# Optimization experiments

Measured on AMD Instinct MI355X. Metric: run time of the kernel, lower is better.

The kernel has to match this reference:

```python
import jax, jax.numpy as jnp
import numpy as np

N_HEAD = 8
D_K = 64
D_V = 512
TOP_K = 64
NEG = jnp.finfo(jnp.float32).min


def setup_inputs() -> dict:
    key = jax.random.key(0)
    ks = jax.random.split(key, 10)
    B, Lq, Lk, E = 2, 2048, 2048, 512
    q = jax.random.normal(ks[0], (B, Lq, E), dtype=jnp.float32)
    k = jax.random.normal(ks[1], (B, Lk, E), dtype=jnp.float32)
    v = jax.random.normal(ks[2], (B, Lk, D_V), dtype=jnp.float32)
    post_softmax_mask = jax.random.randint(ks[3], (B, 1, Lq, Lk), 0, 2, dtype=jnp.int32)
    query_mask_flat = jax.random.uniform(ks[4], (B, Lq), dtype=jnp.float32)
    # Linear weights stored input-major: y = x @ W
    Wq = jax.random.normal(ks[5], (E, N_HEAD * D_K), dtype=jnp.float32) * (E ** -0.5)
    Wk = jax.random.normal(ks[6], (E, N_HEAD * D_K), dtype=jnp.float32) * (E ** -0.5)
    Wv = jax.random.normal(ks[7], (D_V, N_HEAD * D_V), dtype=jnp.float32) * (D_V ** -0.5)
    Wfc = jax.random.normal(ks[8], (N_HEAD * D_V, D_V), dtype=jnp.float32) * ((N_HEAD * D_V) ** -0.5)
    return {"q": q, "k": k, "v": v, "post_softmax_mask": post_softmax_mask,
            "query_mask_flat": query_mask_flat, "Wq": Wq, "Wk": Wk, "Wv": Wv, "Wfc": Wfc}


def _topk_keep_mask(logits, top_k):
    # Scatter True at the per-row top-k indices (matches torch.topk + scatter_).
    B, H, Lq, Lk = logits.shape
    _, idx = jax.lax.top_k(logits, top_k)              # [B,H,Lq,K]
    rows = B * H * Lq
    keep = jnp.zeros((rows, Lk), dtype=bool)
    keep = keep.at[jnp.arange(rows)[:, None], idx.reshape(rows, top_k)].set(True)
    return keep.reshape(B, H, Lq, Lk)


def reference(q, k, v, post_softmax_mask, query_mask_flat, Wq, Wk, Wv, Wfc):
    B, Lq, _ = q.shape
    Lk = k.shape[1]
    q_proj = (q @ Wq).reshape(B, Lq, N_HEAD, D_K).transpose(0, 2, 1, 3)   # [B,H,Lq,dk]
    k_proj = (k @ Wk).reshape(B, Lk, N_HEAD, D_K).transpose(0, 2, 1, 3)   # [B,H,Lk,dk]
    logits = jnp.einsum('bhqd,bhkd->bhqk', q_proj * (D_K ** -0.5), k_proj).astype(jnp.float32)
    # post-softmax mask (applied pre-softmax via -inf fill, as in source)
    logits = jnp.where(post_softmax_mask == 0, NEG, logits)
    # top-k restriction, skipped for rows where query_mask_flat <= 0.5
    keep = _topk_keep_mask(logits, TOP_K)
    masked_queries = (query_mask_flat > 0.5)[:, None, :, None]            # [B,1,Lq,1]
    keep = jnp.where(masked_queries, keep, True)
    logits = jnp.where(keep, logits, NEG)
    attn_probs = jax.nn.softmax(logits, axis=-1).astype(v.dtype)          # [B,H,Lq,Lk]
    v_proj = (v @ Wv).reshape(B, Lk, N_HEAD, D_V).transpose(0, 2, 1, 3)   # [B,H,Lk,dv]
    mixed = jnp.einsum('bhqk,bhkd->bhqd', attn_probs, v_proj)
    output = mixed.transpose(0, 2, 1, 3).reshape(B, Lq, N_HEAD * D_V) @ Wfc
    return output, attn_probs
```

## Files before the change

kernel.cpp:

```cpp
#include <hip/hip_runtime.h>
#include <stdint.h>

#define NEGF  (-3.402823466e38f)
#define TOPK  64

typedef __attribute__((ext_vector_type(8))) short bfrag8;
typedef __attribute__((ext_vector_type(4))) float f32x4;
typedef __attribute__((ext_vector_type(16))) float f32x16;

static __device__ __forceinline__ unsigned short f2bf(float f) {
  union { float f; unsigned u; } c; c.f = f;
  unsigned u = c.u;
  return (unsigned short)((u + 0x7fffu + ((u >> 16) & 1u)) >> 16);
}
static __device__ __forceinline__ unsigned mono(float x) {
  union { float f; unsigned u; } c; c.f = x;
  return (c.u & 0x80000000u) ? ~c.u : (c.u | 0x80000000u);
}
static __device__ __forceinline__ float invmono(unsigned k) {
  union { unsigned u; float f; } c;
  c.u = (k & 0x80000000u) ? (k ^ 0x80000000u) : ~k;
  return c.f;
}
static __device__ __forceinline__ int waveSum(int v) {
  #pragma unroll
  for (int o = 1; o < 64; o <<= 1) v += __shfl_xor(v, o);
  return v;
}
static __device__ __forceinline__ float waveSumF(float v) {
  #pragma unroll
  for (int o = 1; o < 64; o <<= 1) v += __shfl_xor(v, o);
  return v;
}
static __device__ __forceinline__ unsigned waveMaxU(unsigned v) {
  #pragma unroll
  for (int o = 1; o < 64; o <<= 1) {
    unsigned t = (unsigned)__shfl_xor((int)v, o);
    v = v > t ? v : t;
  }
  return v;
}

template<int OBF>
__global__ __launch_bounds__(256) void transpose_k(const float* __restrict__ in,
                                                   void* __restrict__ out, int R, int C) {
  __shared__ float t[32][33];
  int c0 = blockIdx.x * 32, r0 = blockIdx.y * 32;
  int tx = threadIdx.x & 31, ty = (threadIdx.x >> 5) * 4;
  #pragma unroll
  for (int i = 0; i < 4; i++)
    t[ty + i][tx] = in[(size_t)(r0 + ty + i) * C + c0 + tx];
  __syncthreads();
  #pragma unroll
  for (int i = 0; i < 4; i++) {
    float v = t[tx][ty + i];
    size_t idx = (size_t)(c0 + ty + i) * R + r0 + tx;
    if (OBF) ((unsigned short*)out)[idx] = f2bf(v);
    else     ((float*)out)[idx] = v;
  }
}

__global__ __launch_bounds__(256) void proj_f32_kernel(
    const float* __restrict__ q, const float* __restrict__ k,
    const float* __restrict__ WqT, const float* __restrict__ WkT,
    float* __restrict__ qp, float* __restrict__ kp) {
  __shared__ float AsT[64][132];
  __shared__ float BsT[64][132];
  int tid = threadIdx.x;
  int z = blockIdx.z;
  const float* A  = z ? k : q;
  const float* Bt = z ? WkT : WqT;
  float* out      = z ? kp : qp;
  float scale     = z ? 1.0f : 0.125f;
  int m0 = blockIdx.y * 128, n0 = blockIdx.x * 128;
  int lane = tid & 63, w = tid >> 6;
  int lx = lane & 15, ly = lane >> 4;
  int ra = w * 32 + ly * 4;
  int ca = lx * 4;
  int rr = tid >> 1;
  int kq0 = (tid & 1) << 5;
  float acc[8][8] = {};
  for (int k0 = 0; k0 < 512; k0 += 64) {
    const float* ar = A  + (size_t)(m0 + rr) * 512 + k0 + kq0;
    const float* br = Bt + (size_t)(n0 + rr) * 512 + k0 + kq0;
    #pragma unroll
    for (int s = 0; s < 8; s++) {
      float4 av = *(const float4*)(ar + (s << 2));
      float4 bv = *(const float4*)(br + (s << 2));
      int kk = kq0 + (s << 2);
      AsT[kk+0][rr] = av.x; AsT[kk+1][rr] = av.y; AsT[kk+2][rr] = av.z; AsT[kk+3][rr] = av.w;
      BsT[kk+0][rr] = bv.x; BsT[kk+1][rr] = bv.y; BsT[kk+2][rr] = bv.z; BsT[kk+3][rr] = bv.w;
    }
    __syncthreads();
    #pragma unroll 2
    for (int d = 0; d < 64; d++) {
      f32x4 a0 = *(const f32x4*)&AsT[d][ra];
      f32x4 a1 = *(const f32x4*)&AsT[d][ra + 16];
      f32x4 b0 = *(const f32x4*)&BsT[d][ca];
      f32x4 b1 = *(const f32x4*)&BsT[d][ca + 64];
      float a[8] = {a0[0],a0[1],a0[2],a0[3],a1[0],a1[1],a1[2],a1[3]};
      float bb[8] = {b0[0],b0[1],b0[2],b0[3],b1[0],b1[1],b1[2],b1[3]};
      #pragma unroll
      for (int i = 0; i < 8; i++)
        #pragma unroll
        for (int j = 0; j < 8; j++)
          acc[i][j] = fmaf(a[i], bb[j], acc[i][j]);
    }
    __syncthreads();
  }
  #pragma unroll
  for (int i = 0; i < 8; i++) {
    int m = m0 + ra + (i & 3) + ((i >> 2) << 4);
    int b = m >> 11, l = m & 2047;
    #pragma unroll
    for (int half = 0; half < 2; half++) {
      int n = n0 + ca + half * 64;
      int h = n >> 6, dd = n & 63;
      float4 v4;
      v4.x = acc[i][half*4+0]*scale; v4.y = acc[i][half*4+1]*scale;
      v4.z = acc[i][half*4+2]*scale; v4.w = acc[i][half*4+3]*scale;
      *(float4*)(out + ((((size_t)b*8 + h)*2048 + l)*64 + dd)) = v4;
    }
  }
}

__global__ __launch_bounds__(256) void logits_mask_kernel(
    const float* __restrict__ qp, const float* __restrict__ kp,
    const int* __restrict__ mask, float* __restrict__ out) {
  __shared__ float AsT[64][132];
  __shared__ float BsT[64][132];
  int tid = threadIdx.x;
  int z = blockIdx.z, b = z >> 3;
  int m0 = blockIdx.y * 128, n0 = blockIdx.x * 128;
  const float* Ap = qp + (size_t)z * (2048 * 64);
  const float* Bp = kp + (size_t)z * (2048 * 64);
  {
    int rr = tid >> 2;
    int kq = (tid & 3) << 2;
    #pragma unroll
    for (int pass = 0; pass < 2; pass++) {
      int r = rr + (pass << 6);
      const float* ar = Ap + (size_t)(m0 + r) * 64 + kq;
      const float* br = Bp + (size_t)(n0 + r) * 64 + kq;
      #pragma unroll
      for (int s = 0; s < 4; s++) {
        float4 av = *(const float4*)(ar + (s << 4));
        float4 bv = *(const float4*)(br + (s << 4));
        int k = kq + (s << 4);
        AsT[k+0][r] = av.x; AsT[k+1][r] = av.y; AsT[k+2][r] = av.z; AsT[k+3][r] = av.w;
        BsT[k+0][r] = bv.x; BsT[k+1][r] = bv.y; BsT[k+2][r] = bv.z; BsT[k+3][r] = bv.w;
      }
    }
  }
  __syncthreads();
  int lane = tid & 63, w = tid >> 6;
  int lx = lane & 15, ly = lane >> 4;
  int ra = w * 32 + ly * 4;
  int ca = lx * 4;
  float acc[8][8] = {};
  #pragma unroll 2
  for (int d = 0; d < 64; d++) {
    f32x4 a0 = *(const f32x4*)&AsT[d][ra];
    f32x4 a1 = *(const f32x4*)&AsT[d][ra + 16];
    f32x4 b0 = *(const f32x4*)&BsT[d][ca];
    f32x4 b1 = *(const f32x4*)&BsT[d][ca + 64];
    float a[8] = {a0[0],a0[1],a0[2],a0[3],a1[0],a1[1],a1[2],a1[3]};
    float bb[8] = {b0[0],b0[1],b0[2],b0[3],b1[0],b1[1],b1[2],b1[3]};
    #pragma unroll
    for (int i = 0; i < 8; i++)
      #pragma unroll
      for (int j = 0; j < 8; j++)
        acc[i][j] = fmaf(a[i], bb[j], acc[i][j]);
  }
  size_t outbase = (size_t)z * 2048 * 2048;
  const int* mbase = mask + (size_t)b * 2048 * 2048;
  #pragma unroll
  for (int i = 0; i < 8; i++) {
    int row = m0 + ra + (i & 3) + ((i >> 2) << 4);
    const int* mp = mbase + (size_t)row * 2048 + n0;
    float* op = out + outbase + (size_t)row * 2048 + n0;
    int4 mv0 = *(const int4*)(mp + ca);
    int4 mv1 = *(const int4*)(mp + ca + 64);
    float4 o0, o1;
    o0.x = mv0.x ? acc[i][0] : NEGF;
    o0.y = mv0.y ? acc[i][1] : NEGF;
    o0.z = mv0.z ? acc[i][2] : NEGF;
    o0.w = mv0.w ? acc[i][3] : NEGF;
    o1.x = mv1.x ? acc[i][4] : NEGF;
    o1.y = mv1.y ? acc[i][5] : NEGF;
    o1.z = mv1.z ? acc[i][6] : NEGF;
    o1.w = mv1.w ? acc[i][7] : NEGF;
    *(float4*)(op + ca) = o0;
    *(float4*)(op + ca + 64) = o1;
  }
}

__global__ __launch_bounds__(256) void vproj_kernel(const float* __restrict__ v,
    const unsigned short* __restrict__ WvT, unsigned short* __restrict__ vpT) {
  __shared__ unsigned short As[128][64];
  __shared__ unsigned short Bs[128][64];
  int tid = threadIdx.x;
  int lane = tid & 63, wv = tid >> 6;
  int l31 = lane & 31, lh = lane >> 5;
  int wr = wv >> 1, wc = wv & 1;
  int z = blockIdx.z, b = z >> 3, h = z & 7;
  int m0 = blockIdx.y * 128, n0 = blockIdx.x * 128;
  const unsigned short* Ap = WvT + (size_t)(h * 512 + m0) * 512;
  const float* Bp = v + ((size_t)b * 2048 + n0) * 512;
  f32x16 acc[2][2];
  #pragma unroll
  for (int mf = 0; mf < 2; mf++)
    #pragma unroll
    for (int nf = 0; nf < 2; nf++)
      #pragma unroll
      for (int r = 0; r < 16; r++) acc[mf][nf][r] = 0.f;
  int srow = tid >> 1;
  int skc = (tid & 1) << 5;
  for (int k0 = 0; k0 < 512; k0 += 64) {
    {
      const bfrag8* s = (const bfrag8*)(Ap + (size_t)srow * 512 + k0 + skc);
      #pragma unroll
      for (int j = 0; j < 4; j++) {
        int c = (skc >> 3) + j;
        *(bfrag8*)&As[srow][((c + srow) & 7) * 8] = s[j];
      }
    }
    {
      const float* s = Bp + (size_t)srow * 512 + k0 + skc;
      #pragma unroll
      for (int j = 0; j < 4; j++) {
        float4 x0 = *(const float4*)(s + 8*j);
        float4 x1 = *(const float4*)(s + 8*j + 4);
        union { bfrag8 v; unsigned short u[8]; } p;
        p.u[0]=f2bf(x0.x); p.u[1]=f2bf(x0.y); p.u[2]=f2bf(x0.z); p.u[3]=f2bf(x0.w);
        p.u[4]=f2bf(x1.x); p.u[5]=f2bf(x1.y); p.u[6]=f2bf(x1.z); p.u[7]=f2bf(x1.w);
        int c = (skc >> 3) + j;
        *(bfrag8*)&Bs[srow][((c + srow) & 7) * 8] = p.v;
      }
    }
    __syncthreads();
    #pragma unroll
    for (int ks = 0; ks < 4; ks++) {
      int qd = ks * 2 + lh;
      bfrag8 af[2], bfr[2];
      #pragma unroll
      for (int mf = 0; mf < 2; mf++) {
        int r = wr * 64 + mf * 32 + l31;
        af[mf] = *(const bfrag8*)&As[r][((qd + r) & 7) * 8];
      }
      #pragma unroll
      for (int nf = 0; nf < 2; nf++) {
        int n = wc * 64 + nf * 32 + l31;
        bfr[nf] = *(const bfrag8*)&Bs[n][((qd + n) & 7) * 8];
      }
      #pragma unroll
      for (int mf = 0; mf < 2; mf++)
        #pragma unroll
        for (int nf = 0; nf < 2; nf++)
          acc[mf][nf] = __builtin_amdgcn_mfma_f32_32x32x16_bf16(af[mf], bfr[nf], acc[mf][nf], 0, 0, 0);
    }
    __syncthreads();
  }
  #pragma unroll
  for (int mf = 0; mf < 2; mf++)
    #pragma unroll
    for (int nf = 0; nf < 2; nf++) {
      int l = n0 + wc * 64 + nf * 32 + l31;
      #pragma unroll
      for (int r = 0; r < 16; r++) {
        int d = m0 + wr * 64 + mf * 32 + (r & 3) + ((r >> 2) << 3) + (lh << 2);
        vpT[((size_t)z * 512 + d) * 2048 + l] = f2bf(acc[mf][nf][r]);
      }
    }
}

__global__ __launch_bounds__(256) void gemm_bf16_fc(const unsigned short* __restrict__ A,
    const unsigned short* __restrict__ Bt, float* __restrict__ Cout,
    int M, int N, int K) {
  __shared__ unsigned short As[64][72];
  __shared__ unsigned short Bs[128][72];
  int tid = threadIdx.x;
  int lane = tid & 63, wave = tid >> 6;
  int wr = wave >> 1, wc = wave & 1;
  int m0 = blockIdx.y * 64, n0 = blockIdx.x * 128;
  f32x4 acc[2][4];
  #pragma unroll
  for (int mi = 0; mi < 2; mi++)
    #pragma unroll
    for (int ni = 0; ni < 4; ni++) acc[mi][ni] = (f32x4){0.f, 0.f, 0.f, 0.f};
  int arow = tid >> 2, akc = (tid & 3) << 4;
  int brow = tid >> 1, bkc = (tid & 1) << 5;
  for (int k0 = 0; k0 < K; k0 += 64) {
    {
      const bfrag8* s = (const bfrag8*)(A + (size_t)(m0 + arow) * K + k0 + akc);
      *(bfrag8*)&As[arow][akc + 0] = s[0];
      *(bfrag8*)&As[arow][akc + 8] = s[1];
    }
    {
      const bfrag8* s = (const bfrag8*)(Bt + (size_t)(n0 + brow) * K + k0 + bkc);
      #pragma unroll
      for (int j = 0; j < 4; j++)
        *(bfrag8*)&Bs[brow][bkc + 8*j] = s[j];
    }
    __syncthreads();
    #pragma unroll
    for (int kh = 0; kh < 2; kh++) {
      int krd = (kh << 5) + ((lane >> 4) << 3);
      bfrag8 af[2], bfr[4];
      #pragma unroll
      for (int mi = 0; mi < 2; mi++)
        af[mi] = *(const bfrag8*)&As[wr*32 + mi*16 + (lane & 15)][krd];
      #pragma unroll
      for (int ni = 0; ni < 4; ni++)
        bfr[ni] = *(const bfrag8*)&Bs[wc*64 + ni*16 + (lane & 15)][krd];
      #pragma unroll
      for (int mi = 0; mi < 2; mi++)
        #pragma unroll
        for (int ni = 0; ni < 4; ni++)
          acc[mi][ni] = __builtin_amdgcn_mfma_f32_16x16x32_bf16(af[mi], bfr[ni], acc[mi][ni], 0, 0, 0);
    }
    __syncthreads();
  }
  #pragma unroll
  for (int mi = 0; mi < 2; mi++) {
    int rb = m0 + wr*32 + mi*16 + ((lane >> 4) << 2);
    #pragma unroll
    for (int ni = 0; ni < 4; ni++) {
      int col = n0 + wc*64 + ni*16 + (lane & 15);
      f32x4 v = acc[mi][ni];
      #pragma unroll
      for (int j = 0; j < 4; j++)
        Cout[(size_t)(rb + j)*512 + col] = v[j];
    }
  }
}

__global__ __launch_bounds__(512) void pv_kernel(const float* __restrict__ probs,
    const unsigned short* __restrict__ vpT, unsigned short* __restrict__ mixed) {
  __shared__ unsigned short As[64][64];
  __shared__ unsigned short Bs[512][64];
  int tid = threadIdx.x;
  int lane = tid & 63, wv = tid >> 6;
  int l31 = lane & 31, lh = lane >> 5;
  int z = blockIdx.z, m0 = blockIdx.y * 64;
  const float* Ap = probs + (size_t)z * 2048 * 2048 + (size_t)m0 * 2048;
  const unsigned short* Bp = vpT + (size_t)z * 512 * 2048;
  f32x16 acc[2][2];
  #pragma unroll
  for (int mf = 0; mf < 2; mf++)
    #pragma unroll
    for (int nf = 0; nf < 2; nf++)
      #pragma unroll
      for (int r = 0; r < 16; r++) acc[mf][nf][r] = 0.f;
  int a_r = tid >> 3, a_c = tid & 7;
  for (int k0 = 0; k0 < 2048; k0 += 64) {
    {
      const float* s = Ap + (size_t)a_r * 2048 + k0 + a_c * 8;
      float4 x0 = *(const float4*)s;
      float4 x1 = *(const float4*)(s + 4);
      union { bfrag8 v; unsigned short u[8]; } p;
      p.u[0]=f2bf(x0.x); p.u[1]=f2bf(x0.y); p.u[2]=f2bf(x0.z); p.u[3]=f2bf(x0.w);
      p.u[4]=f2bf(x1.x); p.u[5]=f2bf(x1.y); p.u[6]=f2bf(x1.z); p.u[7]=f2bf(x1.w);
      *(bfrag8*)&As[a_r][((a_c + a_r) & 7) * 8] = p.v;
    }
    #pragma unroll
    for (int s = 0; s < 8; s++) {
      int n = (tid >> 3) + (s << 6);
      bfrag8 vb = *(const bfrag8*)(Bp + (size_t)n * 2048 + k0 + a_c * 8);
      *(bfrag8*)&Bs[n][((a_c + n) & 7) * 8] = vb;
    }
    __syncthreads();
    #pragma unroll
    for (int ks = 0; ks < 4; ks++) {
      int qd = ks * 2 + lh;
      bfrag8 af[2], bfr[2];
      #pragma unroll
      for (int mf = 0; mf < 2; mf++) {
        int r = mf * 32 + l31;
        af[mf] = *(const bfrag8*)&As[r][((qd + r) & 7) * 8];
      }
      #pragma unroll
      for (int nf = 0; nf < 2; nf++) {
        int n = wv * 64 + nf * 32 + l31;
        bfr[nf] = *(const bfrag8*)&Bs[n][((qd + n) & 7) * 8];
      }
      #pragma unroll
      for (int mf = 0; mf < 2; mf++)
        #pragma unroll
        for (int nf = 0; nf < 2; nf++)
          acc[mf][nf] = __builtin_amdgcn_mfma_f32_32x32x16_bf16(af[mf], bfr[nf], acc[mf][nf], 0, 0, 0);
    }
    __syncthreads();
  }
  int bb = z >> 3, h = z & 7;
  #pragma unroll
  for (int mf = 0; mf < 2; mf++)
    #pragma unroll
    for (int nf = 0; nf < 2; nf++) {
      int n = wv * 64 + nf * 32 + l31;
      #pragma unroll
      for (int r = 0; r < 16; r++) {
        int row = m0 + mf * 32 + (r & 3) + ((r >> 2) << 3) + (lh << 2);
        mixed[((size_t)bb * 2048 + row) * 4096 + h * 512 + n] = f2bf(acc[mf][nf][r]);
      }
    }
}

__global__ __launch_bounds__(256) void topk_softmax_k(float* __restrict__ probs,
    const float* __restrict__ qmaskf) {
  int lane = threadIdx.x & 63;
  int row = blockIdx.x * 4 + (threadIdx.x >> 6);
  int b = row >> 14, q = row & 2047;
  float* rp = probs + (size_t)row * 2048;
  unsigned key[32];
  #pragma unroll
  for (int j = 0; j < 8; j++) {
    int base = (lane << 2) + (j << 8);
    float4 v = *(const float4*)(rp + base);
    key[4*j+0] = mono(v.x);
    key[4*j+1] = mono(v.y);
    key[4*j+2] = mono(v.z);
    key[4*j+3] = mono(v.w);
  }
  unsigned drop = 0;
  bool qm = qmaskf[b * 2048 + q] > 0.5f;
  if (qm) {
    unsigned lo = 0u, hi = 0xFFFFu;
    while (lo < hi) {
      unsigned mid = lo + ((hi - lo + 1u) >> 1);
      unsigned t = mid << 16;
      int c = 0;
      #pragma unroll
      for (int e = 0; e < 32; e++) c += (key[e] >= t) ? 1 : 0;
      c = waveSum(c);
      if (c >= TOPK) lo = mid; else hi = mid - 1u;
    }
    unsigned P = lo;
    unsigned hiMax = (P << 16) | 0xFFFFu;
    int cgt_hi = 0;
    #pragma unroll
    for (int e = 0; e < 32; e++) cgt_hi += (key[e] > hiMax) ? 1 : 0;
    cgt_hi = waveSum(cgt_hi);
    int remaining = TOPK - cgt_hi;
    unsigned cur = 0xFFFFFFFFu;
    unsigned K64 = P << 16;
    for (;;) {
      unsigned mx = 0;
      #pragma unroll
      for (int e = 0; e < 32; e++) {
        unsigned kk = key[e];
        if ((kk >> 16) == P && kk < cur) mx = mx > kk ? mx : kk;
      }
      mx = waveMaxU(mx);
      int ce = 0;
      #pragma unroll
      for (int e = 0; e < 32; e++) ce += (key[e] == mx) ? 1 : 0;
      ce = waveSum(ce);
      if (remaining <= ce) { K64 = mx; break; }
      remaining -= ce;
      cur = mx;
    }
    int cgt = 0, ceq = 0;
    #pragma unroll
    for (int e = 0; e < 32; e++) { cgt += (key[e] > K64) ? 1 : 0; ceq += (key[e] == K64) ? 1 : 0; }
    cgt = waveSum(cgt);
    int ceqT = waveSum(ceq);
    int r = TOPK - cgt;
    #pragma unroll
    for (int e = 0; e < 32; e++) if (key[e] < K64) drop |= (1u << e);
    if (ceqT > r) {
      int taken = 0;
      for (int j = 0; j < 8; j++) {
        int cl = 0, eqm = 0;
        #pragma unroll
        for (int t = 0; t < 4; t++)
          if (key[4*j+t] == K64) { eqm |= (1 << t); cl++; }
        int incl = cl;
        for (int o = 1; o < 64; o <<= 1) {
          int tt = __shfl_up(incl, o);
          if (lane >= o) incl += tt;
        }
        int pref = incl - cl;
        int tot = __shfl(incl, 63);
        int rk = taken + pref;
        #pragma unroll
        for (int t = 0; t < 4; t++) {
          if ((eqm >> t) & 1) {
            if (rk >= r) drop |= (1u << (4*j+t));
            rk++;
          }
        }
        taken += tot;
      }
    }
  }
  unsigned kmax = 0;
  #pragma unroll
  for (int e = 0; e < 32; e++)
    if (!((drop >> e) & 1u)) kmax = kmax > key[e] ? kmax : key[e];
  kmax = waveMaxU(kmax);
  float mx = invmono(kmax);
  float ex[32]; float s = 0.f;
  #pragma unroll
  for (int e = 0; e < 32; e++) {
    float t = ((drop >> e) & 1u) ? 0.f : __expf(invmono(key[e]) - mx);
    ex[e] = t; s += t;
  }
  s = waveSumF(s);
  float inv = 1.0f / s;
  #pragma unroll
  for (int j = 0; j < 8; j++) {
    int base = (lane << 2) + (j << 8);
    float4 o;
    o.x = ex[4*j+0]*inv; o.y = ex[4*j+1]*inv; o.z = ex[4*j+2]*inv; o.w = ex[4*j+3]*inv;
    *(float4*)(rp + base) = o;
  }
}

extern "C" void kernel_launch(void* const* d_in, const int* in_sizes, int n_in,
                              void* d_out, int out_size, void* d_ws, size_t ws_size,
                              hipStream_t stream) {
  (void)in_sizes; (void)n_in; (void)out_size; (void)ws_size;
  const float* q     = (const float*)d_in[0];
  const float* k     = (const float*)d_in[1];
  const float* v     = (const float*)d_in[2];
  const int*   mask  = (const int*)d_in[3];
  const float* qmask = (const float*)d_in[4];
  const float* Wq    = (const float*)d_in[5];
  const float* Wk    = (const float*)d_in[6];
  const float* Wv    = (const float*)d_in[7];
  const float* Wfc   = (const float*)d_in[8];

  float* out   = (float*)d_out;
  float* probs = out + 2097152;

  char* ws = (char*)d_ws;
  float*          qp    = (float*)(ws + 0);
  float*          kp    = (float*)(ws + 8388608);
  unsigned short* vpT   = (unsigned short*)(ws + 16777216);
  unsigned short* mixed = (unsigned short*)(ws + 50331648);
  float*          WqT   = (float*)(ws + 83886080);
  float*          WkT   = (float*)(ws + 84934656);
  unsigned short* WvT   = (unsigned short*)(ws + 85983232);
  unsigned short* WfcT  = (unsigned short*)(ws + 90177536);

  transpose_k<0><<<dim3(16, 16),  256, 0, stream>>>(Wq,  WqT,  512, 512);
  transpose_k<0><<<dim3(16, 16),  256, 0, stream>>>(Wk,  WkT,  512, 512);
  transpose_k<1><<<dim3(128, 16), 256, 0, stream>>>(Wv,  WvT,  512, 4096);
  transpose_k<1><<<dim3(16, 128), 256, 0, stream>>>(Wfc, WfcT, 4096, 512);

  proj_f32_kernel<<<dim3(4, 32, 2), 256, 0, stream>>>(q, k, WqT, WkT, qp, kp);

  vproj_kernel<<<dim3(16, 4, 16), 256, 0, stream>>>(v, WvT, vpT);

  logits_mask_kernel<<<dim3(16, 16, 16), 256, 0, stream>>>(qp, kp, mask, probs);

  topk_softmax_k<<<dim3(8192), 256, 0, stream>>>(probs, qmask);

  pv_kernel<<<dim3(1, 32, 16), 512, 0, stream>>>(probs, vpT, mixed);

  gemm_bf16_fc<<<dim3(4, 64), 256, 0, stream>>>(mixed, WfcT, out, 4096, 512, 4096);
}
```

Measured before the change: 581.0 us.

## Fuse logits, mask, top-k and softmax into one kernel; remap PV blocks per XCD

Replaces the separate logits+mask kernel and the top-k/softmax kernel with one ltk_kernel. Each block computes full 2048-wide logit rows for 32 queries from a transposed K held in double-buffered LDS, then does the top-k selection and softmax in registers. This removes one full write and read of the 2048x2048x16 float logits tensor in HBM. It also uses ballot/popcount counts, packed bf16 conversion, a reworked FMA loop in the projection, and an XCD-aware block remap for pv_kernel. The cost is a new kpT transpose pass, heavy register pressure (128 logit values per thread) and large shared-memory use, which may limit occupancy.

```diff
diff --git a/kernel.cpp b/kernel.cpp
--- a/kernel.cpp
+++ b/kernel.cpp
@@ -13,6 +13,11 @@
   unsigned u = c.u;
   return (unsigned short)((u + 0x7fffu + ((u >> 16) & 1u)) >> 16);
 }
+static __device__ __forceinline__ unsigned cvtpk_bf16(float lo, float hi) {
+  unsigned r;
+  asm("v_cvt_pk_bf16_f32 %0, %1, %2" : "=v"(r) : "v"(lo), "v"(hi));
+  return r;
+}
 static __device__ __forceinline__ unsigned mono(float x) {
   union { float f; unsigned u; } c; c.f = x;
   return (c.u & 0x80000000u) ? ~c.u : (c.u | 0x80000000u);
@@ -21,11 +26,6 @@
   union { unsigned u; float f; } c;
   c.u = (k & 0x80000000u) ? (k ^ 0x80000000u) : ~k;
   return c.f;
-}
-static __device__ __forceinline__ int waveSum(int v) {
-  #pragma unroll
-  for (int o = 1; o < 64; o <<= 1) v += __shfl_xor(v, o);
-  return v;
 }
 static __device__ __forceinline__ float waveSumF(float v) {
   #pragma unroll
@@ -58,6 +58,23 @@
     if (OBF) ((unsigned short*)out)[idx] = f2bf(v);
     else     ((float*)out)[idx] = v;
   }
+}
+
+__global__ __launch_bounds__(256) void transpose_kp_kernel(const float* __restrict__ kp,
+    float* __restrict__ kpT) {
+  __shared__ float t[32][33];
+  int z = blockIdx.z;
+  const float* in = kp + (size_t)z * 2048 * 64;
+  float* out = kpT + (size_t)z * 64 * 2048;
+  int c0 = blockIdx.x * 32, r0 = blockIdx.y * 32;
+  int tx = threadIdx.x & 31, ty = (threadIdx.x >> 5) * 4;
+  #pragma unroll
+  for (int i = 0; i < 4; i++)
+    t[ty + i][tx] = in[(size_t)(r0 + ty + i) * 64 + c0 + tx];
+  __syncthreads();
+  #pragma unroll
+  for (int i = 0; i < 4; i++)
+    out[(size_t)(c0 + ty + i) * 2048 + r0 + tx] = t[tx][ty + i];
 }
 
 __global__ __launch_bounds__(256) void proj_f32_kernel(
@@ -92,19 +109,22 @@
       BsT[kk+0][rr] = bv.x; BsT[kk+1][rr] = bv.y; BsT[kk+2][rr] = bv.z; BsT[kk+3][rr] = bv.w;
     }
     __syncthreads();
-    #pragma unroll 2
+    #pragma unroll 4
     for (int d = 0; d < 64; d++) {
       f32x4 a0 = *(const f32x4*)&AsT[d][ra];
       f32x4 a1 = *(const f32x4*)&AsT[d][ra + 16];
       f32x4 b0 = *(const f32x4*)&BsT[d][ca];
       f32x4 b1 = *(const f32x4*)&BsT[d][ca + 64];
-      float a[8] = {a0[0],a0[1],a0[2],a0[3],a1[0],a1[1],a1[2],a1[3]};
-      float bb[8] = {b0[0],b0[1],b0[2],b0[3],b1[0],b1[1],b1[2],b1[3]};
-      #pragma unroll
-      for (int i = 0; i < 8; i++)
-        #pragma unroll
-        for (int j = 0; j < 8; j++)
-          acc[i][j] = fmaf(a[i], bb[j], acc[i][j]);
+      #pragma unroll
+      for (int i = 0; i < 4; i++) {
+        #pragma unroll
+        for (int j = 0; j < 4; j++) {
+          acc[i][j]     = fmaf(a0[i], b0[j], acc[i][j]);
+          acc[i][j+4]   = fmaf(a0[i], b1[j], acc[i][j+4]);
+          acc[i+4][j]   = fmaf(a1[i], b0[j], acc[i+4][j]);
+          acc[i+4][j+4] = fmaf(a1[i], b1[j], acc[i+4][j+4]);
+        }
+      }
     }
     __syncthreads();
   }
@@ -124,74 +144,153 @@
   }
 }
 
-__global__ __launch_bounds__(256) void logits_mask_kernel(
-    const float* __restrict__ qp, const float* __restrict__ kp,
-    const int* __restrict__ mask, float* __restrict__ out) {
-  __shared__ float AsT[64][132];
-  __shared__ float BsT[64][132];
+__global__ __launch_bounds__(512, 2) void ltk_kernel(
+    const float* __restrict__ qp, const float* __restrict__ kpT,
+    const int* __restrict__ mask, const float* __restrict__ qmaskf,
+    float* __restrict__ probs) {
+  __shared__ float As[32][68];
+  __shared__ float Bs[2][4 * 2048];
   int tid = threadIdx.x;
-  int z = blockIdx.z, b = z >> 3;
-  int m0 = blockIdx.y * 128, n0 = blockIdx.x * 128;
+  int lane = tid & 63, w = tid >> 6;
+  int z = blockIdx.y, b = z >> 3;
+  int m0 = blockIdx.x * 32;
   const float* Ap = qp + (size_t)z * (2048 * 64);
-  const float* Bp = kp + (size_t)z * (2048 * 64);
+  const float* Bp = kpT + (size_t)z * (64 * 2048);
   {
-    int rr = tid >> 2;
-    int kq = (tid & 3) << 2;
-    #pragma unroll
-    for (int pass = 0; pass < 2; pass++) {
-      int r = rr + (pass << 6);
-      const float* ar = Ap + (size_t)(m0 + r) * 64 + kq;
-      const float* br = Bp + (size_t)(n0 + r) * 64 + kq;
-      #pragma unroll
-      for (int s = 0; s < 4; s++) {
-        float4 av = *(const float4*)(ar + (s << 4));
-        float4 bv = *(const float4*)(br + (s << 4));
-        int k = kq + (s << 4);
-        AsT[k+0][r] = av.x; AsT[k+1][r] = av.y; AsT[k+2][r] = av.z; AsT[k+3][r] = av.w;
-        BsT[k+0][r] = bv.x; BsT[k+1][r] = bv.y; BsT[k+2][r] = bv.z; BsT[k+3][r] = bv.w;
-      }
-    }
-  }
-  __syncthreads();
-  int lane = tid & 63, w = tid >> 6;
-  int lx = lane & 15, ly = lane >> 4;
-  int ra = w * 32 + ly * 4;
-  int ca = lx * 4;
-  float acc[8][8] = {};
-  #pragma unroll 2
-  for (int d = 0; d < 64; d++) {
-    f32x4 a0 = *(const f32x4*)&AsT[d][ra];
-    f32x4 a1 = *(const f32x4*)&AsT[d][ra + 16];
-    f32x4 b0 = *(const f32x4*)&BsT[d][ca];
-    f32x4 b1 = *(const f32x4*)&BsT[d][ca + 64];
-    float a[8] = {a0[0],a0[1],a0[2],a0[3],a1[0],a1[1],a1[2],a1[3]};
-    float bb[8] = {b0[0],b0[1],b0[2],b0[3],b1[0],b1[1],b1[2],b1[3]};
-    #pragma unroll
-    for (int i = 0; i < 8; i++)
-      #pragma unroll
-      for (int j = 0; j < 8; j++)
-        acc[i][j] = fmaf(a[i], bb[j], acc[i][j]);
-  }
-  size_t outbase = (size_t)z * 2048 * 2048;
-  const int* mbase = mask + (size_t)b * 2048 * 2048;
-  #pragma unroll
-  for (int i = 0; i < 8; i++) {
-    int row = m0 + ra + (i & 3) + ((i >> 2) << 4);
-    const int* mp = mbase + (size_t)row * 2048 + n0;
-    float* op = out + outbase + (size_t)row * 2048 + n0;
-    int4 mv0 = *(const int4*)(mp + ca);
-    int4 mv1 = *(const int4*)(mp + ca + 64);
-    float4 o0, o1;
-    o0.x = mv0.x ? acc[i][0] : NEGF;
-    o0.y = mv0.y ? acc[i][1] : NEGF;
-    o0.z = mv0.z ? acc[i][2] : NEGF;
-    o0.w = mv0.w ? acc[i][3] : NEGF;
-    o1.x = mv1.x ? acc[i][4] : NEGF;
-    o1.y = mv1.y ? acc[i][5] : NEGF;
-    o1.z = mv1.z ? acc[i][6] : NEGF;
-    o1.w = mv1.w ? acc[i][7] : NEGF;
-    *(float4*)(op + ca) = o0;
-    *(float4*)(op + ca + 64) = o1;
+    int r = tid >> 4, c4 = (tid & 15) << 2;
+    *(f32x4*)&As[r][c4] = *(const f32x4*)(Ap + (size_t)(m0 + r) * 64 + c4);
+  }
+  int sdd = tid >> 7, sc = (tid & 127) << 2;
+  {
+    #pragma unroll
+    for (int s = 0; s < 4; s++)
+      *(f32x4*)&Bs[0][sdd * 2048 + sc + 512 * s] =
+          *(const f32x4*)(Bp + (size_t)sdd * 2048 + sc + 512 * s);
+  }
+  float lg[4][32];
+  #pragma unroll
+  for (int r = 0; r < 4; r++)
+    #pragma unroll
+    for (int j = 0; j < 32; j++) lg[r][j] = 0.f;
+  int buf = 0;
+  for (int it = 0; it < 16; ++it) {
+    __syncthreads();
+    f32x4 pre0, pre1, pre2, pre3;
+    if (it < 15) {
+      const float* s = Bp + (size_t)(4 * (it + 1) + sdd) * 2048 + sc;
+      pre0 = *(const f32x4*)(s);
+      pre1 = *(const f32x4*)(s + 512);
+      pre2 = *(const f32x4*)(s + 1024);
+      pre3 = *(const f32x4*)(s + 1536);
+    }
+    f32x4 a0 = *(const f32x4*)&As[4*w+0][it * 4];
+    f32x4 a1 = *(const f32x4*)&As[4*w+1][it * 4];
+    f32x4 a2 = *(const f32x4*)&As[4*w+2][it * 4];
+    f32x4 a3 = *(const f32x4*)&As[4*w+3][it * 4];
+    const float* Bb = &Bs[buf][0];
+    #pragma unroll
+    for (int j = 0; j < 32; ++j) {
+      int col = lane + 64 * j;
+      float b0 = Bb[col], b1 = Bb[2048 + col], b2 = Bb[4096 + col], b3 = Bb[6144 + col];
+      lg[0][j] = fmaf(a0[3], b3, fmaf(a0[2], b2, fmaf(a0[1], b1, fmaf(a0[0], b0, lg[0][j]))));
+      lg[1][j] = fmaf(a1[3], b3, fmaf(a1[2], b2, fmaf(a1[1], b1, fmaf(a1[0], b0, lg[1][j]))));
+      lg[2][j] = fmaf(a2[3], b3, fmaf(a2[2], b2, fmaf(a2[1], b1, fmaf(a2[0], b0, lg[2][j]))));
+      lg[3][j] = fmaf(a3[3], b3, fmaf(a3[2], b2, fmaf(a3[1], b1, fmaf(a3[0], b0, lg[3][j]))));
+    }
+    if (it < 15) {
+      float* d = &Bs[buf ^ 1][sdd * 2048 + sc];
+      *(f32x4*)(d)        = pre0;
+      *(f32x4*)(d + 512)  = pre1;
+      *(f32x4*)(d + 1024) = pre2;
+      *(f32x4*)(d + 1536) = pre3;
+    }
+    buf ^= 1;
+  }
+  int bbase = b * 2048;
+  #pragma unroll
+  for (int r = 0; r < 4; ++r) {
+    int row = m0 + 4 * w + r;
+    const int* mp = mask + ((size_t)bbase + row) * 2048;
+    unsigned key[32];
+    #pragma unroll
+    for (int j = 0; j < 32; ++j) {
+      int mm = mp[lane + 64 * j];
+      key[j] = mono(mm ? lg[r][j] : NEGF);
+    }
+    bool qm = qmaskf[bbase + row] > 0.5f;
+    unsigned drop = 0;
+    if (qm) {
+      unsigned lo = 0u, hi = 0xFFFFu;
+      while (lo < hi) {
+        unsigned mid = lo + ((hi - lo + 1u) >> 1);
+        unsigned t = mid << 16;
+        int c = 0;
+        #pragma unroll
+        for (int e = 0; e < 32; e++) c += __popcll(__ballot(key[e] >= t));
+        if (c >= TOPK) lo = mid; else hi = mid - 1u;
+      }
+      unsigned P = lo;
+      unsigned hiMax = (P << 16) | 0xFFFFu;
+      int cgt_hi = 0;
+      #pragma unroll
+      for (int e = 0; e < 32; e++) cgt_hi += __popcll(__ballot(key[e] > hiMax));
+      int remaining = TOPK - cgt_hi;
+      unsigned cur = 0xFFFFFFFFu;
+      unsigned K64 = P << 16;
+      for (;;) {
+        unsigned mx = 0;
+        #pragma unroll
+        for (int e = 0; e < 32; e++) {
+          unsigned kk = key[e];
+          if ((kk >> 16) == P && kk < cur) mx = mx > kk ? mx : kk;
+        }
+        mx = waveMaxU(mx);
+        int ce = 0;
+        #pragma unroll
+        for (int e = 0; e < 32; e++) ce += __popcll(__ballot(key[e] == mx));
+        if (remaining <= ce) { K64 = mx; break; }
+        remaining -= ce;
+        cur = mx;
+      }
+      int cgt = 0, ceqT = 0;
+      #pragma unroll
+      for (int e = 0; e < 32; e++) {
+        cgt  += __popcll(__ballot(key[e] > K64));
+        ceqT += __popcll(__ballot(key[e] == K64));
+      }
+      int rneed = TOPK - cgt;
+      #pragma unroll
+      for (int e = 0; e < 32; e++) if (key[e] < K64) drop |= (1u << e);
+      if (ceqT > rneed) {
+        int taken = 0;
+        unsigned long long lmask = (lane == 63) ? 0xFFFFFFFFFFFFFFFFull >> 1
+                                                : ((1ull << lane) - 1ull);
+        for (int j = 0; j < 32; ++j) {
+          bool eq = (key[j] == K64);
+          unsigned long long bal = __ballot(eq);
+          int pref = __popcll(bal & ((lane == 63) ? ~(1ull << 63) : ((1ull << lane) - 1ull)));
+          if (eq && (taken + pref) >= rneed) drop |= (1u << j);
+          taken += __popcll(bal);
+        }
+        (void)lmask;
+      }
+    }
+    unsigned kmax = 0;
+    #pragma unroll
+    for (int e = 0; e < 32; e++)
+      if (!((drop >> e) & 1u)) kmax = kmax > key[e] ? kmax : key[e];
+    kmax = waveMaxU(kmax);
+    float mx = invmono(kmax);
+    float ssum = 0.f;
+    #pragma unroll
+    for (int e = 0; e < 32; e++)
+      if (!((drop >> e) & 1u)) ssum += __expf(invmono(key[e]) - mx);
+    ssum = waveSumF(ssum);
+    float inv = 1.0f / ssum;
+    float* op = probs + ((size_t)z * 2048 + row) * 2048;
+    #pragma unroll
+    for (int j = 0; j < 32; ++j)
+      op[lane + 64 * j] = ((drop >> j) & 1u) ? 0.f : __expf(invmono(key[j]) - mx) * inv;
   }
 }
 
@@ -231,9 +330,9 @@
       for (int j = 0; j < 4; j++) {
         float4 x0 = *(const float4*)(s + 8*j);
         float4 x1 = *(const float4*)(s + 8*j + 4);
-        union { bfrag8 v; unsigned short u[8]; } p;
-        p.u[0]=f2bf(x0.x); p.u[1]=f2bf(x0.y); p.u[2]=f2bf(x0.z); p.u[3]=f2bf(x0.w);
-        p.u[4]=f2bf(x1.x); p.u[5]=f2bf(x1.y); p.u[6]=f2bf(x1.z); p.u[7]=f2bf(x1.w);
+        union { bfrag8 v; unsigned w[4]; } p;
+        p.w[0] = cvtpk_bf16(x0.x, x0.y); p.w[1] = cvtpk_bf16(x0.z, x0.w);
+        p.w[2] = cvtpk_bf16(x1.x, x1.y); p.w[3] = cvtpk_bf16(x1.z, x1.w);
         int c = (skc >> 3) + j;
         *(bfrag8*)&Bs[srow][((c + srow) & 7) * 8] = p.v;
       }
@@ -342,7 +441,10 @@
   int tid = threadIdx.x;
   int lane = tid & 63, wv = tid >> 6;
   int l31 = lane & 31, lh = lane >> 5;
-  int z = blockIdx.z, m0 = blockIdx.y * 64;
+  int bid = blockIdx.x;
+  int xcd = bid & 7, idx = bid >> 3;
+  int z = (xcd << 1) | (idx >> 5);
+  int m0 = (idx & 31) << 6;
   const float* Ap = probs + (size_t)z * 2048 * 2048 + (size_t)m0 * 2048;
   const unsigned short* Bp = vpT + (size_t)z * 512 * 2048;
   f32x16 acc[2][2];
@@ -358,9 +460,9 @@
       const float* s = Ap + (size_t)a_r * 2048 + k0 + a_c * 8;
       float4 x0 = *(const float4*)s;
       float4 x1 = *(const float4*)(s + 4);
-      union { bfrag8 v; unsigned short u[8]; } p;
-      p.u[0]=f2bf(x0.x); p.u[1]=f2bf(x0.y); p.u[2]=f2bf(x0.z); p.u[3]=f2bf(x0.w);
-      p.u[4]=f2bf(x1.x); p.u[5]=f2bf(x1.y); p.u[6]=f2bf(x1.z); p.u[7]=f2bf(x1.w);
+      union { bfrag8 v; unsigned w[4]; } p;
+      p.w[0] = cvtpk_bf16(x0.x, x0.y); p.w[1] = cvtpk_bf16(x0.z, x0.w);
+      p.w[2] = cvtpk_bf16(x1.x, x1.y); p.w[3] = cvtpk_bf16(x1.z, x1.w);
       *(bfrag8*)&As[a_r][((a_c + a_r) & 7) * 8] = p.v;
     }
     #pragma unroll
@@ -404,117 +506,6 @@
         mixed[((size_t)bb * 2048 + row) * 4096 + h * 512 + n] = f2bf(acc[mf][nf][r]);
       }
     }
-}
-
-__global__ __launch_bounds__(256) void topk_softmax_k(float* __restrict__ probs,
-    const float* __restrict__ qmaskf) {
-  int lane = threadIdx.x & 63;
-  int row = blockIdx.x * 4 + (threadIdx.x >> 6);
-  int b = row >> 14, q = row & 2047;
-  float* rp = probs + (size_t)row * 2048;
-  unsigned key[32];
-  #pragma unroll
-  for (int j = 0; j < 8; j++) {
-    int base = (lane << 2) + (j << 8);
-    float4 v = *(const float4*)(rp + base);
-    key[4*j+0] = mono(v.x);
-    key[4*j+1] = mono(v.y);
-    key[4*j+2] = mono(v.z);
-    key[4*j+3] = mono(v.w);
-  }
-  unsigned drop = 0;
-  bool qm = qmaskf[b * 2048 + q] > 0.5f;
-  if (qm) {
-    unsigned lo = 0u, hi = 0xFFFFu;
-    while (lo < hi) {
-      unsigned mid = lo + ((hi - lo + 1u) >> 1);
-      unsigned t = mid << 16;
-      int c = 0;
-      #pragma unroll
-      for (int e = 0; e < 32; e++) c += (key[e] >= t) ? 1 : 0;
-      c = waveSum(c);
-      if (c >= TOPK) lo = mid; else hi = mid - 1u;
-    }
-    unsigned P = lo;
-    unsigned hiMax = (P << 16) | 0xFFFFu;
-    int cgt_hi = 0;
-    #pragma unroll
-    for (int e = 0; e < 32; e++) cgt_hi += (key[e] > hiMax) ? 1 : 0;
-    cgt_hi = waveSum(cgt_hi);
-    int remaining = TOPK - cgt_hi;
-    unsigned cur = 0xFFFFFFFFu;
-    unsigned K64 = P << 16;
-    for (;;) {
-      unsigned mx = 0;
-      #pragma unroll
-      for (int e = 0; e < 32; e++) {
-        unsigned kk = key[e];
-        if ((kk >> 16) == P && kk < cur) mx = mx > kk ? mx : kk;
-      }
-      mx = waveMaxU(mx);
-      int ce = 0;
-      #pragma unroll
-      for (int e = 0; e < 32; e++) ce += (key[e] == mx) ? 1 : 0;
-      ce = waveSum(ce);
-      if (remaining <= ce) { K64 = mx; break; }
-      remaining -= ce;
-      cur = mx;
-    }
-    int cgt = 0, ceq = 0;
-    #pragma unroll
-    for (int e = 0; e < 32; e++) { cgt += (key[e] > K64) ? 1 : 0; ceq += (key[e] == K64) ? 1 : 0; }
-    cgt = waveSum(cgt);
-    int ceqT = waveSum(ceq);
-    int r = TOPK - cgt;
-    #pragma unroll
-    for (int e = 0; e < 32; e++) if (key[e] < K64) drop |= (1u << e);
-    if (ceqT > r) {
-      int taken = 0;
-      for (int j = 0; j < 8; j++) {
-        int cl = 0, eqm = 0;
-        #pragma unroll
-        for (int t = 0; t < 4; t++)
-          if (key[4*j+t] == K64) { eqm |= (1 << t); cl++; }
-        int incl = cl;
-        for (int o = 1; o < 64; o <<= 1) {
-          int tt = __shfl_up(incl, o);
-          if (lane >= o) incl += tt;
-        }
-        int pref = incl - cl;
-        int tot = __shfl(incl, 63);
-        int rk = taken + pref;
-        #pragma unroll
-        for (int t = 0; t < 4; t++) {
-          if ((eqm >> t) & 1) {
-            if (rk >= r) drop |= (1u << (4*j+t));
-            rk++;
-          }
-        }
-        taken += tot;
-      }
-    }
-  }
-  unsigned kmax = 0;
-  #pragma unroll
-  for (int e = 0; e < 32; e++)
-    if (!((drop >> e) & 1u)) kmax = kmax > key[e] ? kmax : key[e];
-  kmax = waveMaxU(kmax);
-  float mx = invmono(kmax);
-  float ex[32]; float s = 0.f;
-  #pragma unroll
-  for (int e = 0; e < 32; e++) {
-    float t = ((drop >> e) & 1u) ? 0.f : __expf(invmono(key[e]) - mx);
-    ex[e] = t; s += t;
-  }
-  s = waveSumF(s);
-  float inv = 1.0f / s;
-  #pragma unroll
-  for (int j = 0; j < 8; j++) {
-    int base = (lane << 2) + (j << 8);
-    float4 o;
-    o.x = ex[4*j+0]*inv; o.y = ex[4*j+1]*inv; o.z = ex[4*j+2]*inv; o.w = ex[4*j+3]*inv;
-    *(float4*)(rp + base) = o;
-  }
 }
 
 extern "C" void kernel_launch(void* const* d_in, const int* in_sizes, int n_in,
@@ -539,6 +530,7 @@
   float*          kp    = (float*)(ws + 8388608);
   unsigned short* vpT   = (unsigned short*)(ws + 16777216);
   unsigned short* mixed = (unsigned short*)(ws + 50331648);
+  float*          kpT   = (float*)(ws + 50331648);
   float*          WqT   = (float*)(ws + 83886080);
   float*          WkT   = (float*)(ws + 84934656);
   unsigned short* WvT   = (unsigned short*)(ws + 85983232);
@@ -551,13 +543,13 @@
 
   proj_f32_kernel<<<dim3(4, 32, 2), 256, 0, stream>>>(q, k, WqT, WkT, qp, kp);
 
+  transpose_kp_kernel<<<dim3(2, 64, 16), 256, 0, stream>>>(kp, kpT);
+
   vproj_kernel<<<dim3(16, 4, 16), 256, 0, stream>>>(v, WvT, vpT);
 
-  logits_mask_kernel<<<dim3(16, 16, 16), 256, 0, stream>>>(qp, kp, mask, probs);
-
-  topk_softmax_k<<<dim3(8192), 256, 0, stream>>>(probs, qmask);
-
-  pv_kernel<<<dim3(1, 32, 16), 512, 0, stream>>>(probs, vpT, mixed);
+  ltk_kernel<<<dim3(64, 16), 512, 0, stream>>>(qp, kpT, mask, qmask, probs);
+
+  pv_kernel<<<dim3(512), 512, 0, stream>>>(probs, vpT, mixed);
 
   gemm_bf16_fc<<<dim3(4, 64), 256, 0, stream>>>(mixed, WfcT, out, 4096, 512, 4096);
 }
```

Result: slower. 838.6 us (+44.3%).
